# Performance work log

Measured on AMD Instinct MI355X. Metric: run time of the kernel, lower is better.

## Reference

```python
import jax, jax.numpy as jnp
import numpy as np

V = 32000          # output_dim / num_embeddings
E = 1024           # embedding_dim == hidden_size
NL = 2             # num_layers
EOS_IDX = V - 1
EPS = 1e-3
LOG_BOUND = float(np.log(1.0 - EPS))
B, T = 4, 512


def setup_inputs() -> dict:
    key = jax.random.key(0)
    ks = jax.random.split(key, 12)
    s = 1.0 / np.sqrt(E)
    inp = {
        "tokens": jax.random.randint(ks[0], (B, T), 0, V, dtype=jnp.int32),
        "emb": jax.random.normal(ks[1], (V, E), jnp.float32) * 0.02,
        "Wproj": jax.random.normal(ks[2], (V, E), jnp.float32) * 0.02,
    }
    for l in range(NL):
        inp[f"Wih{l}"] = jax.random.uniform(ks[3 + 4 * l], (4 * E, E), jnp.float32, -s, s)
        inp[f"Whh{l}"] = jax.random.uniform(ks[4 + 4 * l], (4 * E, E), jnp.float32, -s, s)
        inp[f"bih{l}"] = jax.random.uniform(ks[5 + 4 * l], (4 * E,), jnp.float32, -s, s)
        inp[f"bhh{l}"] = jax.random.uniform(ks[6 + 4 * l], (4 * E,), jnp.float32, -s, s)
    return inp


def _lstm_layer(x, Wih, Whh, bih, bhh):
    # x: [T, B, E] -> [T, B, H], PyTorch gate order i,f,g,o
    Bsz, H = x.shape[1], Whh.shape[1]
    b = bih + bhh

    def step(carry, xt):
        h, c = carry
        g = xt @ Wih.T + h @ Whh.T + b          # [B, 4H]
        i, f, gg, o = jnp.split(g, 4, axis=-1)
        c = jax.nn.sigmoid(f) * c + jax.nn.sigmoid(i) * jnp.tanh(gg)
        h = jax.nn.sigmoid(o) * jnp.tanh(c)
        return (h, c), h

    h0 = jnp.zeros((Bsz, H), x.dtype)
    _, hs = jax.lax.scan(step, (h0, h0), x)
    return hs


def _forward(tokens, emb, Wih0, Whh0, bih0, bhh0, Wih1, Whh1, bih1, bhh1, Wproj):
    x = emb[tokens]                              # [B, T, E]
    h = jnp.swapaxes(x, 0, 1)                    # [T, B, E]
    h = _lstm_layer(h, Wih0, Whh0, bih0, bhh0)
    h = _lstm_layer(h, Wih1, Whh1, bih1, bhh1)
    h_all = jnp.swapaxes(h, 0, 1)                # [B, T, E]
    logits = h_all @ Wproj.T                     # [B, T, V]

    v_lprobs = jax.nn.log_softmax(logits[..., :EOS_IDX], axis=-1)  # [B,T,V-1]
    eos_logits = logits[..., EOS_IDX:EOS_IDX + 1]                  # [B,T,1]

    # cumsum of constant log(1-eps) over time -> (t+1)*log(1-eps)
    t = jnp.arange(1, T + 1, dtype=logits.dtype)
    log_lb = (t * LOG_BOUND)[None, :, None]                        # [1,T,1]
    f_lower_bound = 1.0 - jnp.exp(log_lb)

    log_eos_ub = jax.nn.log_sigmoid(eos_logits)
    log_eos_lb = jax.nn.log_sigmoid(-eos_logits)

    v_lprobs = log_lb + log_eos_lb + v_lprobs
    log_lb_eos = jnp.log(f_lower_bound) + log_eos_lb
    # log(a+b) = log(a) - log(sigmoid(log(a) - log(b)))
    lprob_eos = log_lb_eos - jax.nn.log_sigmoid(log_lb_eos - log_eos_ub)

    log_ps = jnp.concatenate([v_lprobs, lprob_eos], axis=-1)       # [B,T,V]
    log_ps = log_ps - jax.nn.logsumexp(log_ps, axis=-1, keepdims=True)
    return log_ps


def reference(tokens, emb, Wih0, Whh0, bih0, bhh0, Wih1, Whh1, bih1, bhh1, Wproj):
    return _forward(tokens, emb, Wih0, Whh0, bih0, bhh0, Wih1, Whh1, bih1, bhh1, Wproj)
```

## Files before the change

### kernel.cpp

```cpp
#include <hip/hip_runtime.h>
#include <cstddef>

#define BB 4
#define TT 512
#define EE 1024
#define G4 4096
#define VV 32000
#define EOSI 31999
#define LOG_BOUND (-1.0005003335835335e-3f)
#define NBLK 256

__device__ __forceinline__ float softplusf(float x) {
  return fmaxf(x, 0.0f) + log1pf(expf(-fabsf(x)));
}
__device__ __forceinline__ float sigmoidf(float x) {
  return 1.0f / (1.0f + expf(-x));
}

__global__ void init_state(unsigned* flag0, unsigned* flag1) {
  int i = threadIdx.x;
  flag0[i] = 0u;
  flag1[i] = 0u;
}

__global__ __launch_bounds__(256) void gemm_nt(
    const float* __restrict__ A, const float* __restrict__ Bw,
    float* __restrict__ C, int M, int N, int K,
    const float* __restrict__ bias1, const float* __restrict__ bias2,
    const int* __restrict__ tokens, int mode)
{
  __shared__ float As[16][132];
  __shared__ float Bs[16][132];
  const int tid  = threadIdx.x;
  const int bcol = blockIdx.x * 128;
  const int brow = blockIdx.y * 128;

  const int idx0 = tid, idx1 = tid + 256;
  const int ar0 = idx0 >> 2, ak0 = (idx0 & 3) * 4;
  const int ar1 = idx1 >> 2, ak1 = (idx1 & 3) * 4;

  long arow0, arow1;
  {
    int m0 = brow + ar0, m1 = brow + ar1;
    if (mode == 1) {
      arow0 = tokens[((m0 & 3) << 9) + (m0 >> 2)];
      arow1 = tokens[((m1 & 3) << 9) + (m1 >> 2)];
    } else if (mode == 2) {
      arow0 = ((m0 & 511) << 2) + (m0 >> 9) + 4;
      arow1 = ((m1 & 511) << 2) + (m1 >> 9) + 4;
    } else {
      arow0 = m0; arow1 = m1;
    }
  }
  const long brw0 = bcol + ar0, brw1 = bcol + ar1;

  float acc[8][8];
  #pragma unroll
  for (int i = 0; i < 8; ++i)
    #pragma unroll
    for (int j = 0; j < 8; ++j) acc[i][j] = 0.f;

  const int ti = tid >> 4, tj = tid & 15;

  for (int k0 = 0; k0 < K; k0 += 16) {
    float4 a0 = *(const float4*)(A  + arow0 * (long)K + k0 + ak0);
    float4 a1 = *(const float4*)(A  + arow1 * (long)K + k0 + ak1);
    float4 b0 = *(const float4*)(Bw + brw0  * (long)K + k0 + ak0);
    float4 b1 = *(const float4*)(Bw + brw1  * (long)K + k0 + ak1);
    __syncthreads();
    As[ak0+0][ar0] = a0.x; As[ak0+1][ar0] = a0.y; As[ak0+2][ar0] = a0.z; As[ak0+3][ar0] = a0.w;
    As[ak1+0][ar1] = a1.x; As[ak1+1][ar1] = a1.y; As[ak1+2][ar1] = a1.z; As[ak1+3][ar1] = a1.w;
    Bs[ak0+0][ar0] = b0.x; Bs[ak0+1][ar0] = b0.y; Bs[ak0+2][ar0] = b0.z; Bs[ak0+3][ar0] = b0.w;
    Bs[ak1+0][ar1] = b1.x; Bs[ak1+1][ar1] = b1.y; Bs[ak1+2][ar1] = b1.z; Bs[ak1+3][ar1] = b1.w;
    __syncthreads();
    #pragma unroll
    for (int kk = 0; kk < 16; ++kk) {
      float af[8], bf[8];
      #pragma unroll
      for (int i = 0; i < 8; ++i) af[i] = As[kk][ti*8 + i];
      #pragma unroll
      for (int j = 0; j < 8; ++j) bf[j] = Bs[kk][tj*8 + j];
      #pragma unroll
      for (int i = 0; i < 8; ++i)
        #pragma unroll
        for (int j = 0; j < 8; ++j) acc[i][j] += af[i] * bf[j];
    }
  }

  float bv[8];
  #pragma unroll
  for (int jj = 0; jj < 8; ++jj) {
    int n = bcol + tj*8 + jj;
    float bb = 0.f;
    if (bias1) bb += bias1[n];
    if (bias2) bb += bias2[n];
    bv[jj] = bb;
  }
  #pragma unroll
  for (int i = 0; i < 8; ++i) {
    int m = brow + ti*8 + i;
    float* cp = C + (size_t)m * N + bcol + tj*8;
    float4 v0 = make_float4(acc[i][0]+bv[0], acc[i][1]+bv[1], acc[i][2]+bv[2], acc[i][3]+bv[3]);
    float4 v1 = make_float4(acc[i][4]+bv[4], acc[i][5]+bv[5], acc[i][6]+bv[6], acc[i][7]+bv[7]);
    *(float4*)cp = v0;
    *(float4*)(cp + 4) = v1;
  }
}

__global__ __launch_bounds__(256, 1) void lstm_persist(
    const float* __restrict__ gpre,
    const float* __restrict__ Whh,
    float* __restrict__ hseq,
    unsigned* __restrict__ flag)
{
  __shared__ float hlds[4096];
  __shared__ float gsum[16][4];

  const int tid = threadIdx.x;
  const int bid = blockIdx.x;
  const int rl = tid >> 4, ks = tid & 15;

  float4 wreg[16];
  {
    const int grow = (rl >> 2) * 1024 + bid * 4 + (rl & 3);
    const float4* wrow = (const float4*)(Whh + (size_t)grow * 1024);
    #pragma unroll
    for (int i = 0; i < 16; ++i) wreg[i] = wrow[i * 16 + ks];
  }
  {
    float4* h4 = (float4*)hlds;
    #pragma unroll
    for (int i = 0; i < 4; ++i) h4[tid + 256 * i] = make_float4(0.f, 0.f, 0.f, 0.f);
  }
  float creg = 0.f;
  float gpv0 = 0.f, gpv1 = 0.f, gpv2 = 0.f, gpv3 = 0.f;
  const int gb = tid >> 2, gj = tid & 3;
  if (tid < 16) {
    const float* gp = gpre + (size_t)gb * 4096 + bid * 4 + gj;
    gpv0 = gp[0]; gpv1 = gp[1024]; gpv2 = gp[2048]; gpv3 = gp[3072];
  }
  __syncthreads();

  const float4* hl4 = (const float4*)hlds;

  for (int t = 0; t < TT; ++t) {
    float a0 = 0.f, a1 = 0.f, a2 = 0.f, a3 = 0.f;
    #pragma unroll
    for (int i = 0; i < 16; ++i) {
      const int k4 = i * 16 + ks;
      float4 w  = wreg[i];
      float4 h0 = hl4[k4];
      float4 h1 = hl4[256 + k4];
      float4 h2 = hl4[512 + k4];
      float4 h3 = hl4[768 + k4];
      a0 += w.x*h0.x + w.y*h0.y + w.z*h0.z + w.w*h0.w;
      a1 += w.x*h1.x + w.y*h1.y + w.z*h1.z + w.w*h1.w;
      a2 += w.x*h2.x + w.y*h2.y + w.z*h2.z + w.w*h2.w;
      a3 += w.x*h3.x + w.y*h3.y + w.z*h3.z + w.w*h3.w;
    }
    #pragma unroll
    for (int m = 8; m >= 1; m >>= 1) {
      a0 += __shfl_xor(a0, m, 64);
      a1 += __shfl_xor(a1, m, 64);
      a2 += __shfl_xor(a2, m, 64);
      a3 += __shfl_xor(a3, m, 64);
    }
    if (ks == 0) *(float4*)&gsum[rl][0] = make_float4(a0, a1, a2, a3);
    __syncthreads();

    if (tid < 16) {
      float gi = gpv0 + gsum[     gj][gb];
      float gf = gpv1 + gsum[ 4 + gj][gb];
      float gg = gpv2 + gsum[ 8 + gj][gb];
      float go = gpv3 + gsum[12 + gj][gb];
      float c = sigmoidf(gf) * creg + sigmoidf(gi) * tanhf(gg);
      creg = c;
      float hv = sigmoidf(go) * tanhf(c);
      __hip_atomic_store(hseq + (size_t)(t + 1) * G4 + gb * 1024 + bid * 4 + gj,
                         hv, __ATOMIC_RELAXED, __HIP_MEMORY_SCOPE_AGENT);
    }

    if (t == TT - 1) break;

    if (tid < 64) {
      asm volatile("s_waitcnt vmcnt(0)" ::: "memory");
      if (tid == 0)
        __hip_atomic_store(flag + bid, (unsigned)(t + 1),
                           __ATOMIC_RELAXED, __HIP_MEMORY_SCOPE_AGENT);
      if (tid < 16) {
        const float* gp = gpre + (size_t)(t + 1) * 16384 + (size_t)gb * 4096 + bid * 4 + gj;
        gpv0 = gp[0]; gpv1 = gp[1024]; gpv2 = gp[2048]; gpv3 = gp[3072];
        asm volatile("" ::: "memory");
      }
      const unsigned tgt = (unsigned)(t + 1);
      for (;;) {
        unsigned f0 = __hip_atomic_load(flag + tid,       __ATOMIC_RELAXED, __HIP_MEMORY_SCOPE_AGENT);
        unsigned f1 = __hip_atomic_load(flag + tid +  64, __ATOMIC_RELAXED, __HIP_MEMORY_SCOPE_AGENT);
        unsigned f2 = __hip_atomic_load(flag + tid + 128, __ATOMIC_RELAXED, __HIP_MEMORY_SCOPE_AGENT);
        unsigned f3 = __hip_atomic_load(flag + tid + 192, __ATOMIC_RELAXED, __HIP_MEMORY_SCOPE_AGENT);
        if (__all((f0 >= tgt) && (f1 >= tgt) && (f2 >= tgt) && (f3 >= tgt))) break;
      }
    }
    __syncthreads();

    {
      const unsigned long long* hs =
          (const unsigned long long*)(hseq + (size_t)(t + 1) * G4);
      unsigned long long* hd = (unsigned long long*)hlds;
      #pragma unroll
      for (int i = 0; i < 8; ++i)
        hd[tid + 256 * i] = __hip_atomic_load(hs + tid + 256 * i,
                                              __ATOMIC_RELAXED, __HIP_MEMORY_SCOPE_AGENT);
    }
    __syncthreads();
  }
}

__global__ __launch_bounds__(256) void row_stats(
    const float* __restrict__ logits, float* __restrict__ rowA, float* __restrict__ rowE)
{
  const int m = blockIdx.x;
  const float* row = logits + (size_t)m * VV;
  __shared__ float red[8];
  const int tid = threadIdx.x;

  float mx = -3.0e38f;
  for (int v = tid; v < EOSI; v += 256) mx = fmaxf(mx, row[v]);
  for (int off = 32; off; off >>= 1) mx = fmaxf(mx, __shfl_down(mx, off, 64));
  if ((tid & 63) == 0) red[tid >> 6] = mx;
  __syncthreads();
  if (tid == 0) red[4] = fmaxf(fmaxf(red[0], red[1]), fmaxf(red[2], red[3]));
  __syncthreads();
  mx = red[4];

  float s = 0.f;
  for (int v = tid; v < EOSI; v += 256) s += expf(row[v] - mx);
  for (int off = 32; off; off >>= 1) s += __shfl_down(s, off, 64);
  if ((tid & 63) == 0) red[tid >> 6] = s;
  __syncthreads();

  if (tid == 0) {
    s = red[0] + red[1] + red[2] + red[3];
    float lse_v = mx + logf(s);
    float eos = row[EOSI];
    int t = m & 511;
    float log_lb = (float)(t + 1) * LOG_BOUND;
    float log_eos_lb = -softplusf(eos);
    float log_eos_ub = -softplusf(-eos);
    float shift = log_lb + log_eos_lb;
    float f_lb = -expm1f(log_lb);
    float log_lb_eos = logf(f_lb) + log_eos_lb;
    float lprob_eos = log_lb_eos + softplusf(log_eos_ub - log_lb_eos);
    float aa = shift, bb = lprob_eos;
    float lse2 = fmaxf(aa, bb) + log1pf(expf(-fabsf(aa - bb)));
    rowA[m] = lse_v + lse2 - shift;
    rowE[m] = lprob_eos - lse2;
  }
}

__global__ __launch_bounds__(256) void finalize(
    float* __restrict__ out, const float* __restrict__ rowA, const float* __restrict__ rowE)
{
  const int m = blockIdx.y;
  const int v4 = blockIdx.x * 256 + threadIdx.x;
  if (v4 >= 8000) return;
  float4* rp = (float4*)(out + (size_t)m * VV);
  const float A = rowA[m];
  float4 p = rp[v4];
  p.x -= A; p.y -= A; p.z -= A; p.w -= A;
  if (v4 == 7999) p.w = rowE[m];
  rp[v4] = p;
}

extern "C" void kernel_launch(void* const* d_in, const int* in_sizes, int n_in,
                              void* d_out, int out_size, void* d_ws, size_t ws_size,
                              hipStream_t stream)
{
  const int*   tokens = (const int*)  d_in[0];
  const float* emb    = (const float*)d_in[1];
  const float* Wproj  = (const float*)d_in[2];
  const float* Wih0   = (const float*)d_in[3];
  const float* Whh0   = (const float*)d_in[4];
  const float* bih0   = (const float*)d_in[5];
  const float* bhh0   = (const float*)d_in[6];
  const float* Wih1   = (const float*)d_in[7];
  const float* Whh1   = (const float*)d_in[8];
  const float* bih1   = (const float*)d_in[9];
  const float* bhh1   = (const float*)d_in[10];
  float* out = (float*)d_out;

  float* ws = (float*)d_ws;
  float* g0   = ws;
  float* g1   = g0 + (size_t)2048*4096;
  float* h0   = g1 + (size_t)2048*4096;
  float* h1   = h0 + (size_t)513*4096;
  unsigned* flag0 = (unsigned*)(h1 + (size_t)513*4096);
  unsigned* flag1 = flag0 + 256;
  float* rowA = (float*)(flag1 + 256);
  float* rowE = rowA + 2048;

  init_state<<<1, 256, 0, stream>>>(flag0, flag1);

  gemm_nt<<<dim3(32, 16), 256, 0, stream>>>(emb, Wih0, g0, 2048, 4096, 1024,
                                            bih0, bhh0, tokens, 1);
  lstm_persist<<<NBLK, 256, 0, stream>>>(g0, Whh0, h0, flag0);

  gemm_nt<<<dim3(32, 16), 256, 0, stream>>>(h0 + 4096, Wih1, g1, 2048, 4096, 1024,
                                            bih1, bhh1, nullptr, 0);
  lstm_persist<<<NBLK, 256, 0, stream>>>(g1, Whh1, h1, flag1);

  gemm_nt<<<dim3(250, 16), 256, 0, stream>>>(h1, Wproj, out, 2048, 32000, 1024,
                                             nullptr, nullptr, nullptr, 2);

  row_stats<<<2048, 256, 0, stream>>>(out, rowA, rowE);
  finalize<<<dim3(32, 2048), 256, 0, stream>>>(out, rowA, rowE);
}
```

Before: 10.18 ms.

## Fuse both LSTM layers into one wavefront-pipelined persistent kernel

Replaces the two sequential persistent LSTM launches and the intermediate layer-1 input GEMM with a single persistent kernel. Layer 1 runs one timestep behind layer 0, and it computes its input projection on the fly from the layer-0 hidden state already held in LDS. This cuts the number of serialized grid-wide barriers from roughly 1024 to 513 and removes a GEMM launch. In exchange, each block keeps three weight slices in registers (Whh0, Wih1, Whh1), which raises register pressure, and each step does three times the recurrent matvec work. The flag polling is also spread across all 256 threads.

After: 15.28 ms. 1.5x slower.

```diff
diff --git a/kernel.cpp b/kernel.cpp
--- a/kernel.cpp
+++ b/kernel.cpp
@@ -17,10 +17,8 @@
   return 1.0f / (1.0f + expf(-x));
 }
 
-__global__ void init_state(unsigned* flag0, unsigned* flag1) {
-  int i = threadIdx.x;
-  flag0[i] = 0u;
-  flag1[i] = 0u;
+__global__ void init_state(unsigned* flag) {
+  flag[threadIdx.x] = 0u;
 }
 
 __global__ __launch_bounds__(256) void gemm_nt(
@@ -107,110 +105,171 @@
   }
 }
 
-__global__ __launch_bounds__(256, 1) void lstm_persist(
-    const float* __restrict__ gpre,
-    const float* __restrict__ Whh,
-    float* __restrict__ hseq,
+__global__ __launch_bounds__(256, 1) void lstm2_persist(
+    const float* __restrict__ g0pre,
+    const float* __restrict__ Whh0,
+    const float* __restrict__ Wih1,
+    const float* __restrict__ Whh1,
+    const float* __restrict__ bih1,
+    const float* __restrict__ bhh1,
+    float* __restrict__ h0seq,
+    float* __restrict__ h1seq,
     unsigned* __restrict__ flag)
 {
-  __shared__ float hlds[4096];
-  __shared__ float gsum[16][4];
+  __shared__ float hl0[4096];
+  __shared__ float hl1[4096];
+  __shared__ float gsum[48][4];
 
   const int tid = threadIdx.x;
   const int bid = blockIdx.x;
   const int rl = tid >> 4, ks = tid & 15;
-
-  float4 wreg[16];
+  const int grow = (rl >> 2) * 1024 + bid * 4 + (rl & 3);
+
+  float4 w0[16], wi1[16], wh1[16];
   {
-    const int grow = (rl >> 2) * 1024 + bid * 4 + (rl & 3);
-    const float4* wrow = (const float4*)(Whh + (size_t)grow * 1024);
-    #pragma unroll
-    for (int i = 0; i < 16; ++i) wreg[i] = wrow[i * 16 + ks];
+    const float4* r0 = (const float4*)(Whh0 + (size_t)grow * 1024);
+    const float4* r1 = (const float4*)(Wih1 + (size_t)grow * 1024);
+    const float4* r2 = (const float4*)(Whh1 + (size_t)grow * 1024);
+    #pragma unroll
+    for (int i = 0; i < 16; ++i) {
+      w0[i]  = r0[i * 16 + ks];
+      wi1[i] = r1[i * 16 + ks];
+      wh1[i] = r2[i * 16 + ks];
+    }
   }
   {
-    float4* h4 = (float4*)hlds;
-    #pragma unroll
-    for (int i = 0; i < 4; ++i) h4[tid + 256 * i] = make_float4(0.f, 0.f, 0.f, 0.f);
-  }
+    float4 z = make_float4(0.f, 0.f, 0.f, 0.f);
+    float4* a = (float4*)hl0; float4* b = (float4*)hl1;
+    #pragma unroll
+    for (int i = 0; i < 4; ++i) { a[tid + 256*i] = z; b[tid + 256*i] = z; }
+  }
+
   float creg = 0.f;
+  const int q = tid & 15, gb = q >> 2, gj = q & 3;
   float gpv0 = 0.f, gpv1 = 0.f, gpv2 = 0.f, gpv3 = 0.f;
-  const int gb = tid >> 2, gj = tid & 3;
+  float bs0 = 0.f, bs1 = 0.f, bs2 = 0.f, bs3 = 0.f;
   if (tid < 16) {
-    const float* gp = gpre + (size_t)gb * 4096 + bid * 4 + gj;
+    const float* gp = g0pre + (size_t)gb * 4096 + bid * 4 + gj;
     gpv0 = gp[0]; gpv1 = gp[1024]; gpv2 = gp[2048]; gpv3 = gp[3072];
+  } else if (tid < 32) {
+    int o = bid * 4 + gj;
+    bs0 = bih1[o]        + bhh1[o];
+    bs1 = bih1[1024 + o] + bhh1[1024 + o];
+    bs2 = bih1[2048 + o] + bhh1[2048 + o];
+    bs3 = bih1[3072 + o] + bhh1[3072 + o];
   }
   __syncthreads();
 
-  const float4* hl4 = (const float4*)hlds;
-
-  for (int t = 0; t < TT; ++t) {
-    float a0 = 0.f, a1 = 0.f, a2 = 0.f, a3 = 0.f;
+  const float4* h04 = (const float4*)hl0;
+  const float4* h14 = (const float4*)hl1;
+
+  for (int tt = 0; tt <= 512; ++tt) {
+    float a00=0.f,a01=0.f,a02=0.f,a03=0.f;
+    float a10=0.f,a11=0.f,a12=0.f,a13=0.f;
+    float a20=0.f,a21=0.f,a22=0.f,a23=0.f;
     #pragma unroll
     for (int i = 0; i < 16; ++i) {
       const int k4 = i * 16 + ks;
-      float4 w  = wreg[i];
-      float4 h0 = hl4[k4];
-      float4 h1 = hl4[256 + k4];
-      float4 h2 = hl4[512 + k4];
-      float4 h3 = hl4[768 + k4];
-      a0 += w.x*h0.x + w.y*h0.y + w.z*h0.z + w.w*h0.w;
-      a1 += w.x*h1.x + w.y*h1.y + w.z*h1.z + w.w*h1.w;
-      a2 += w.x*h2.x + w.y*h2.y + w.z*h2.z + w.w*h2.w;
-      a3 += w.x*h3.x + w.y*h3.y + w.z*h3.z + w.w*h3.w;
+      float4 x0 = h04[k4], x1 = h04[256+k4], x2 = h04[512+k4], x3 = h04[768+k4];
+      float4 y0 = h14[k4], y1 = h14[256+k4], y2 = h14[512+k4], y3 = h14[768+k4];
+      float4 w = w0[i];
+      a00 += w.x*x0.x + w.y*x0.y + w.z*x0.z + w.w*x0.w;
+      a01 += w.x*x1.x + w.y*x1.y + w.z*x1.z + w.w*x1.w;
+      a02 += w.x*x2.x + w.y*x2.y + w.z*x2.z + w.w*x2.w;
+      a03 += w.x*x3.x + w.y*x3.y + w.z*x3.z + w.w*x3.w;
+      w = wi1[i];
+      a10 += w.x*x0.x + w.y*x0.y + w.z*x0.z + w.w*x0.w;
+      a11 += w.x*x1.x + w.y*x1.y + w.z*x1.z + w.w*x1.w;
+      a12 += w.x*x2.x + w.y*x2.y + w.z*x2.z + w.w*x2.w;
+      a13 += w.x*x3.x + w.y*x3.y + w.z*x3.z + w.w*x3.w;
+      w = wh1[i];
+      a20 += w.x*y0.x + w.y*y0.y + w.z*y0.z + w.w*y0.w;
+      a21 += w.x*y1.x + w.y*y1.y + w.z*y1.z + w.w*y1.w;
+      a22 += w.x*y2.x + w.y*y2.y + w.z*y2.z + w.w*y2.w;
+      a23 += w.x*y3.x + w.y*y3.y + w.z*y3.z + w.w*y3.w;
     }
     #pragma unroll
     for (int m = 8; m >= 1; m >>= 1) {
-      a0 += __shfl_xor(a0, m, 64);
-      a1 += __shfl_xor(a1, m, 64);
-      a2 += __shfl_xor(a2, m, 64);
-      a3 += __shfl_xor(a3, m, 64);
-    }
-    if (ks == 0) *(float4*)&gsum[rl][0] = make_float4(a0, a1, a2, a3);
+      a00 += __shfl_xor(a00, m, 64); a01 += __shfl_xor(a01, m, 64);
+      a02 += __shfl_xor(a02, m, 64); a03 += __shfl_xor(a03, m, 64);
+      a10 += __shfl_xor(a10, m, 64); a11 += __shfl_xor(a11, m, 64);
+      a12 += __shfl_xor(a12, m, 64); a13 += __shfl_xor(a13, m, 64);
+      a20 += __shfl_xor(a20, m, 64); a21 += __shfl_xor(a21, m, 64);
+      a22 += __shfl_xor(a22, m, 64); a23 += __shfl_xor(a23, m, 64);
+    }
+    if (ks == 0) {
+      *(float4*)&gsum[     rl][0] = make_float4(a00, a01, a02, a03);
+      *(float4*)&gsum[16 + rl][0] = make_float4(a10, a11, a12, a13);
+      *(float4*)&gsum[32 + rl][0] = make_float4(a20, a21, a22, a23);
+    }
     __syncthreads();
 
     if (tid < 16) {
-      float gi = gpv0 + gsum[     gj][gb];
-      float gf = gpv1 + gsum[ 4 + gj][gb];
-      float gg = gpv2 + gsum[ 8 + gj][gb];
-      float go = gpv3 + gsum[12 + gj][gb];
-      float c = sigmoidf(gf) * creg + sigmoidf(gi) * tanhf(gg);
-      creg = c;
-      float hv = sigmoidf(go) * tanhf(c);
-      __hip_atomic_store(hseq + (size_t)(t + 1) * G4 + gb * 1024 + bid * 4 + gj,
-                         hv, __ATOMIC_RELAXED, __HIP_MEMORY_SCOPE_AGENT);
-    }
-
-    if (t == TT - 1) break;
+      if (tt < 512) {
+        float gi = gpv0 + gsum[     gj][gb];
+        float gf = gpv1 + gsum[ 4 + gj][gb];
+        float gg = gpv2 + gsum[ 8 + gj][gb];
+        float go = gpv3 + gsum[12 + gj][gb];
+        float c = sigmoidf(gf) * creg + sigmoidf(gi) * tanhf(gg);
+        creg = c;
+        float hv = sigmoidf(go) * tanhf(c);
+        __hip_atomic_store(h0seq + (size_t)(tt + 1) * G4 + gb * 1024 + bid * 4 + gj,
+                           hv, __ATOMIC_RELAXED, __HIP_MEMORY_SCOPE_AGENT);
+      }
+    } else if (tid < 32) {
+      if (tt >= 1) {
+        float gi = bs0 + gsum[16 + gj][gb] + gsum[32 + gj][gb];
+        float gf = bs1 + gsum[20 + gj][gb] + gsum[36 + gj][gb];
+        float gg = bs2 + gsum[24 + gj][gb] + gsum[40 + gj][gb];
+        float go = bs3 + gsum[28 + gj][gb] + gsum[44 + gj][gb];
+        float c = sigmoidf(gf) * creg + sigmoidf(gi) * tanhf(gg);
+        creg = c;
+        float hv = sigmoidf(go) * tanhf(c);
+        __hip_atomic_store(h1seq + (size_t)tt * G4 + gb * 1024 + bid * 4 + gj,
+                           hv, __ATOMIC_RELAXED, __HIP_MEMORY_SCOPE_AGENT);
+      }
+    }
+
+    if (tt == 512) break;
 
     if (tid < 64) {
       asm volatile("s_waitcnt vmcnt(0)" ::: "memory");
       if (tid == 0)
-        __hip_atomic_store(flag + bid, (unsigned)(t + 1),
+        __hip_atomic_store(flag + bid, (unsigned)(tt + 1),
                            __ATOMIC_RELAXED, __HIP_MEMORY_SCOPE_AGENT);
-      if (tid < 16) {
-        const float* gp = gpre + (size_t)(t + 1) * 16384 + (size_t)gb * 4096 + bid * 4 + gj;
-        gpv0 = gp[0]; gpv1 = gp[1024]; gpv2 = gp[2048]; gpv3 = gp[3072];
-        asm volatile("" ::: "memory");
+    }
+    if (tid < 16 && tt + 1 < 512) {
+      const float* gp = g0pre + (size_t)(tt + 1) * 16384 + (size_t)gb * 4096 + bid * 4 + gj;
+      gpv0 = gp[0]; gpv1 = gp[1024]; gpv2 = gp[2048]; gpv3 = gp[3072];
+      asm volatile("" ::: "memory");
+    }
+    {
+      const unsigned tgt = (unsigned)(tt + 1);
+      for (;;) {
+        unsigned f = __hip_atomic_load(flag + tid, __ATOMIC_RELAXED, __HIP_MEMORY_SCOPE_AGENT);
+        if (__all(f >= tgt)) break;
       }
-      const unsigned tgt = (unsigned)(t + 1);
-      for (;;) {
-        unsigned f0 = __hip_atomic_load(flag + tid,       __ATOMIC_RELAXED, __HIP_MEMORY_SCOPE_AGENT);
-        unsigned f1 = __hip_atomic_load(flag + tid +  64, __ATOMIC_RELAXED, __HIP_MEMORY_SCOPE_AGENT);
-        unsigned f2 = __hip_atomic_load(flag + tid + 128, __ATOMIC_RELAXED, __HIP_MEMORY_SCOPE_AGENT);
-        unsigned f3 = __hip_atomic_load(flag + tid + 192, __ATOMIC_RELAXED, __HIP_MEMORY_SCOPE_AGENT);
-        if (__all((f0 >= tgt) && (f1 >= tgt) && (f2 >= tgt) && (f3 >= tgt))) break;
-      }
-    }
+    }
+    asm volatile("" ::: "memory");
     __syncthreads();
 
     {
-      const unsigned long long* hs =
-          (const unsigned long long*)(hseq + (size_t)(t + 1) * G4);
-      unsigned long long* hd = (unsigned long long*)hlds;
+      const unsigned long long* s0 =
+          (const unsigned long long*)(h0seq + (size_t)(tt + 1) * G4);
+      unsigned long long* d0 = (unsigned long long*)hl0;
       #pragma unroll
       for (int i = 0; i < 8; ++i)
-        hd[tid + 256 * i] = __hip_atomic_load(hs + tid + 256 * i,
+        d0[tid + 256*i] = __hip_atomic_load(s0 + tid + 256*i,
+                                            __ATOMIC_RELAXED, __HIP_MEMORY_SCOPE_AGENT);
+      if (tt >= 1) {
+        const unsigned long long* s1 =
+            (const unsigned long long*)(h1seq + (size_t)tt * G4);
+        unsigned long long* d1 = (unsigned long long*)hl1;
+        #pragma unroll
+        for (int i = 0; i < 8; ++i)
+          d1[tid + 256*i] = __hip_atomic_load(s1 + tid + 256*i,
                                               __ATOMIC_RELAXED, __HIP_MEMORY_SCOPE_AGENT);
+      }
     }
     __syncthreads();
   }
@@ -291,23 +350,19 @@
 
   float* ws = (float*)d_ws;
   float* g0   = ws;
-  float* g1   = g0 + (size_t)2048*4096;
-  float* h0   = g1 + (size_t)2048*4096;
+  float* h0   = g0 + (size_t)2048*4096;
   float* h1   = h0 + (size_t)513*4096;
-  unsigned* flag0 = (unsigned*)(h1 + (size_t)513*4096);
-  unsigned* flag1 = flag0 + 256;
-  float* rowA = (float*)(flag1 + 256);
+  unsigned* flag = (unsigned*)(h1 + (size_t)513*4096);
+  float* rowA = (float*)(flag + 256);
   float* rowE = rowA + 2048;
 
-  init_state<<<1, 256, 0, stream>>>(flag0, flag1);
+  init_state<<<1, 256, 0, stream>>>(flag);
 
   gemm_nt<<<dim3(32, 16), 256, 0, stream>>>(emb, Wih0, g0, 2048, 4096, 1024,
                                             bih0, bhh0, tokens, 1);
-  lstm_persist<<<NBLK, 256, 0, stream>>>(g0, Whh0, h0, flag0);
-
-  gemm_nt<<<dim3(32, 16), 256, 0, stream>>>(h0 + 4096, Wih1, g1, 2048, 4096, 1024,
-                                            bih1, bhh1, nullptr, 0);
-  lstm_persist<<<NBLK, 256, 0, stream>>>(g1, Whh1, h1, flag1);
+
+  lstm2_persist<<<NBLK, 256, 0, stream>>>(g0, Whh0, Wih1, Whh1, bih1, bhh1,
+                                          h0, h1, flag);
 
   gemm_nt<<<dim3(250, 16), 256, 0, stream>>>(h1, Wproj, out, 2048, 32000, 1024,
                                              nullptr, nullptr, nullptr, 2);
```
